# Optimization experiments

Hardware: AMD Instinct MI355X
Metric: run time of the kernel (lower is better)

Reference implementation:

```python
import jax, jax.numpy as jnp
import numpy as np

B, T, C = 8, 2048, 1024  # micro_bsz, seq_len, n_embd (== complexsize)


def setup_inputs() -> dict:
    key = jax.random.key(0)
    ks = jax.random.split(key, 6)
    w = lambda k, shape: (jax.random.normal(k, shape, dtype=jnp.float32) * 0.02)
    return {
        "x": jax.random.normal(ks[0], (B, T, C), dtype=jnp.float32),
        "Wk": w(ks[1], (2 * C, C)),      # key: n_embd -> 2*n_embd (no bias)
        "Wa": w(ks[2], (C, 2 * C)),      # activation: 2*n_embd -> n_embd (no bias)
        "Wf": w(ks[3], (2, C, C)),       # WaveNet filter conv, kernel=2, WIO layout
        "Wg": w(ks[4], (2, C, C)),       # WaveNet gate conv, kernel=2, WIO layout
        "Wo": w(ks[5], (C, C)),          # WaveNet 1x1 output projection
    }


def _causal_conv(x, W):
    # x: [B,T,Cin], W: [K,Cin,Cout]; left-pad K-1 for causality
    return jax.lax.conv_general_dilated(
        x, W, window_strides=(1,), padding=[(W.shape[0] - 1, 0)],
        dimension_numbers=("NWC", "WIO", "NWC"))


def _wavenet_short(x, Wf, Wg, Wo):
    # undialated gated WaveNet unit: tanh(conv_f(x)) * sigmoid(conv_g(x)) -> 1x1 proj
    h = jnp.tanh(_causal_conv(x, Wf)) * jax.nn.sigmoid(_causal_conv(x, Wg))
    return h @ Wo.T


def reference(x, Wk, Wa, Wf, Wg, Wo):
    Bx, Tx, Cx = x.shape
    k = (x @ Wk.T).reshape(Bx, Tx, Cx, 2)                 # [B,T,C,2]
    cv = jax.lax.complex(k[..., 0], k[..., 1])            # view_as_complex -> [B,T,C]
    scale = jax.lax.cummax(jnp.abs(cv), axis=1)           # running max of magnitude
    cv2 = cv / scale.astype(cv.dtype)                      # normalize magnitude <= 1
    kv = jnp.cumprod(cv2, axis=1)                          # complex cumulative product
    re = jnp.stack([kv.real, kv.imag], axis=-1).reshape(Bx, Tx, 2 * Cx)  # view_as_real
    return (re @ Wa.T) * _wavenet_short(x * scale, Wf, Wg, Wo)
```

## Files before the change

### kernel.cpp

```cpp
#include <hip/hip_runtime.h>
#include <cmath>

#define T_SEQ 2048
#define C_DIM 1024
#define BM 128
#define BN 128
#define BK 32

typedef unsigned short u16;
typedef unsigned int u32;
typedef short bf16x8 __attribute__((ext_vector_type(8)));
typedef _Float16 f16x8 __attribute__((ext_vector_type(8)));
typedef float f32x4 __attribute__((ext_vector_type(4)));
typedef unsigned short u16x8 __attribute__((ext_vector_type(8)));

#define AS1 __attribute__((address_space(1)))
#define AS3 __attribute__((address_space(3)))

__device__ __forceinline__ u16 f2bf(float f) {
    u32 u = __builtin_bit_cast(u32, f);
    u32 r = u + 0x7fffu + ((u >> 16) & 1u);
    return (u16)(r >> 16);
}
__device__ __forceinline__ u16 f2h(float f) {
    return __builtin_bit_cast(u16, (_Float16)f);
}
__device__ __forceinline__ float h2f(u16 h) {
    return (float)__builtin_bit_cast(_Float16, h);
}
__device__ __forceinline__ void gl_lds16(const void* g, void* l) {
    __builtin_amdgcn_global_load_lds((const AS1 u32*)g, (AS3 u32*)l, 16, 0, 0);
}

__device__ __forceinline__ int xcd_swz(int lin, int nwg) {
    return (lin & 7) * (nwg >> 3) + (lin >> 3);
}

template<int ASTAGE, int EPI, int DT>
__global__ __launch_bounds__(256)
void mfma_gemm(const void* __restrict__ Abase, const u16* __restrict__ B0,
               void* __restrict__ Cout, int M, int N, int K)
{
    __shared__ u16 lds[2 * 2 * 4096];
    const int tid  = threadIdx.x;
    const int lane = tid & 63;
    const int wid  = tid >> 6;
    const int wr = wid >> 1, wc = wid & 1;
    const int gx = gridDim.x;
    const int lin = xcd_swz(blockIdx.x + gx * blockIdx.y, gx * gridDim.y);
    const int m0 = (lin / gx) * BM;
    const int n0 = (lin % gx) * BN;
    const int NT = K / BK;

    f32x4 acc[4][4] = {};

    auto stage = [&](int it, int buf) {
        const int k0 = it * BK;
        u16* base = &lds[buf * 8192];
        #pragma unroll
        for (int i = 0; i < 2; ++i) {
            const int chunk = wid + 4 * i;
            const int rloc  = chunk * 16 + (lane >> 2);
            const int slot  = (lane & 3) ^ ((rloc >> 1) & 3);
            gl_lds16(B0 + (size_t)(n0 + rloc) * K + k0 + slot * 8,
                     base + 4096 + chunk * 512);
        }
        if constexpr (ASTAGE == 0) {
            const u16* Ap = (const u16*)Abase;
            #pragma unroll
            for (int i = 0; i < 2; ++i) {
                const int chunk = wid + 4 * i;
                const int rloc  = chunk * 16 + (lane >> 2);
                const int slot = (lane & 3) ^ ((rloc >> 1) & 3);
                gl_lds16(Ap + (size_t)(m0 + rloc) * K + k0 + slot * 8,
                         base + chunk * 512);
            }
        } else {
            const float* Af = (const float*)Abase;
            const int r = tid >> 1, h = tid & 1;
            const float* src = Af + (size_t)(m0 + r) * K + k0 + h * 16;
            const float4 q0 = ((const float4*)src)[0];
            const float4 q1 = ((const float4*)src)[1];
            const float4 q2 = ((const float4*)src)[2];
            const float4 q3 = ((const float4*)src)[3];
            float v[16] = {q0.x,q0.y,q0.z,q0.w, q1.x,q1.y,q1.z,q1.w,
                           q2.x,q2.y,q2.z,q2.w, q3.x,q3.y,q3.z,q3.w};
            const int rb = r * 32;
            #pragma unroll
            for (int s2 = 0; s2 < 2; ++s2) {
                const int slot = 2 * h + s2;
                const int sp = slot ^ ((r >> 1) & 3);
                u16x8 w;
                #pragma unroll
                for (int j = 0; j < 8; ++j) w[j] = f2bf(v[s2 * 8 + j]);
                *(u16x8*)&base[rb + sp * 8] = w;
            }
        }
    };

    auto compute = [&](int buf) {
        const u16* base = &lds[buf * 8192];
        if constexpr (DT == 0) {
            bf16x8 a[4], b[4];
            #pragma unroll
            for (int f = 0; f < 4; ++f) {
                const int row = wr * 64 + f * 16 + (lane & 15);
                const int sp  = ((lane >> 4) & 3) ^ ((row >> 1) & 3);
                a[f] = *(const bf16x8*)&base[row * 32 + sp * 8];
                const int rowb = wc * 64 + f * 16 + (lane & 15);
                const int spb  = ((lane >> 4) & 3) ^ ((rowb >> 1) & 3);
                b[f] = *(const bf16x8*)&base[4096 + rowb * 32 + spb * 8];
            }
            #pragma unroll
            for (int fm = 0; fm < 4; ++fm)
                #pragma unroll
                for (int fn = 0; fn < 4; ++fn)
                    acc[fm][fn] = __builtin_amdgcn_mfma_f32_16x16x32_bf16(a[fm], b[fn], acc[fm][fn], 0, 0, 0);
        } else {
            f16x8 a[4], b[4];
            #pragma unroll
            for (int f = 0; f < 4; ++f) {
                const int row = wr * 64 + f * 16 + (lane & 15);
                const int sp  = ((lane >> 4) & 3) ^ ((row >> 1) & 3);
                a[f] = *(const f16x8*)&base[row * 32 + sp * 8];
                const int rowb = wc * 64 + f * 16 + (lane & 15);
                const int spb  = ((lane >> 4) & 3) ^ ((rowb >> 1) & 3);
                b[f] = *(const f16x8*)&base[4096 + rowb * 32 + spb * 8];
            }
            #pragma unroll
            for (int fm = 0; fm < 4; ++fm)
                #pragma unroll
                for (int fn = 0; fn < 4; ++fn)
                    acc[fm][fn] = __builtin_amdgcn_mfma_f32_16x16x32_f16(a[fm], b[fn], acc[fm][fn], 0, 0, 0);
        }
    };

    stage(0, 0);
    int cur = 0;
    for (int it = 0; it < NT; ++it) {
        __syncthreads();
        if (it + 1 < NT) stage(it + 1, cur ^ 1);
        compute(cur);
        cur ^= 1;
    }

    const int crow0 = m0 + wr * 64 + ((lane >> 4) << 2);
    const int ccol  = n0 + wc * 64 + (lane & 15);
    #pragma unroll
    for (int fm = 0; fm < 4; ++fm)
        #pragma unroll
        for (int fn = 0; fn < 4; ++fn)
            #pragma unroll
            for (int r = 0; r < 4; ++r) {
                const size_t idx = (size_t)(crow0 + fm * 16 + r) * N + ccol + fn * 16;
                if constexpr (EPI == 0)      ((float*)Cout)[idx] = acc[fm][fn][r];
                else if constexpr (EPI == 1) ((float*)Cout)[idx] *= acc[fm][fn][r];
                else                         ((u16*)Cout)[idx] = f2h(acc[fm][fn][r]);
            }
}

__global__ __launch_bounds__(256)
void conv_gate(const u16* __restrict__ A, const u16* __restrict__ Wfgt,
               u16* __restrict__ H, int M)
{
    constexpr int KIT = C_DIM / BK;
    constexpr int NT  = 2 * KIT;
    __shared__ u16 lds[2 * 3 * 4096];
    const int tid  = threadIdx.x;
    const int lane = tid & 63;
    const int wid  = tid >> 6;
    const int wr = wid >> 1, wc = wid & 1;
    const int gx = gridDim.x;
    const int lin = xcd_swz(blockIdx.x + gx * blockIdx.y, gx * gridDim.y);
    const int m0 = (lin / gx) * BM;
    const int n0 = (lin % gx) * BN;

    f32x4 accF[4][4] = {};
    f32x4 accG[4][4] = {};

    auto stage = [&](int it, int buf) {
        const int p  = it / KIT;
        const int k0 = (it - p * KIT) * BK;
        u16* base = &lds[buf * 12288];
        const u16* BF = Wfgt + (size_t)p * 2 * C_DIM * C_DIM;
        const u16* BG = BF + (size_t)C_DIM * C_DIM;
        const int sh = (p == 0) ? 1 : 0;
        #pragma unroll
        for (int i = 0; i < 2; ++i) {
            const int chunk = wid + 4 * i;
            const int rloc  = chunk * 16 + (lane >> 2);
            const int slot  = (lane & 3) ^ ((rloc >> 1) & 3);
            int grow = m0 + rloc - sh;
            if (grow < 0) grow = 0;
            gl_lds16(A + (size_t)grow * C_DIM + k0 + slot * 8,
                     base + chunk * 512);
            gl_lds16(BF + (size_t)(n0 + rloc) * C_DIM + k0 + slot * 8,
                     base + 4096 + chunk * 512);
            gl_lds16(BG + (size_t)(n0 + rloc) * C_DIM + k0 + slot * 8,
                     base + 8192 + chunk * 512);
        }
    };

    auto compute = [&](int buf) {
        const u16* base = &lds[buf * 12288];
        bf16x8 a[4], bf[4], bg[4];
        #pragma unroll
        for (int f = 0; f < 4; ++f) {
            const int row = wr * 64 + f * 16 + (lane & 15);
            const int sp  = ((lane >> 4) & 3) ^ ((row >> 1) & 3);
            a[f] = *(const bf16x8*)&base[row * 32 + sp * 8];
            const int rowb = wc * 64 + f * 16 + (lane & 15);
            const int spb  = ((lane >> 4) & 3) ^ ((rowb >> 1) & 3);
            bf[f] = *(const bf16x8*)&base[4096 + rowb * 32 + spb * 8];
            bg[f] = *(const bf16x8*)&base[8192 + rowb * 32 + spb * 8];
        }
        #pragma unroll
        for (int fm = 0; fm < 4; ++fm)
            #pragma unroll
            for (int fn = 0; fn < 4; ++fn) {
                accF[fm][fn] = __builtin_amdgcn_mfma_f32_16x16x32_bf16(a[fm], bf[fn], accF[fm][fn], 0, 0, 0);
                accG[fm][fn] = __builtin_amdgcn_mfma_f32_16x16x32_bf16(a[fm], bg[fn], accG[fm][fn], 0, 0, 0);
            }
    };

    stage(0, 0);
    int cur = 0;
    for (int it = 0; it < NT; ++it) {
        __syncthreads();
        if ((it / KIT) == 0 && (m0 % T_SEQ) == 0) {
            if (tid < 4) {
                u16x8 z = {0,0,0,0,0,0,0,0};
                *(u16x8*)&lds[cur * 12288 + tid * 8] = z;
            }
            __syncthreads();
        }
        if (it + 1 < NT) stage(it + 1, cur ^ 1);
        compute(cur);
        cur ^= 1;
    }

    const int crow0 = m0 + wr * 64 + ((lane >> 4) << 2);
    const int ccol  = n0 + wc * 64 + (lane & 15);
    #pragma unroll
    for (int fm = 0; fm < 4; ++fm)
        #pragma unroll
        for (int fn = 0; fn < 4; ++fn)
            #pragma unroll
            for (int r = 0; r < 4; ++r) {
                const float fv = accF[fm][fn][r];
                const float gv = accG[fm][fn][r];
                const float th = 1.0f - 2.0f / (expf(2.0f * fv) + 1.0f);
                const float sg = 1.0f / (1.0f + expf(-gv));
                H[(size_t)(crow0 + fm * 16 + r) * C_DIM + ccol + fn * 16] = f2bf(th * sg);
            }
}

#define SSEG 32
#define SCHB 32
#define SSL (T_SEQ / SSEG)

__global__ __launch_bounds__(1024, 1)
void scan_kernel(u16* __restrict__ kq, const float* __restrict__ x,
                 u16* __restrict__ yb)
{
    __shared__ float  lmax[SSEG][SCHB];
    __shared__ float2 lprod[SSEG][SCHB];
    const int blk = blockIdx.x;
    const int b   = blk >> 5;
    const int c0  = (blk & 31) * SCHB;
    const int ch  = threadIdx.x & (SCHB - 1);
    const int seg = threadIdx.x >> 5;
    const int c   = c0 + ch;
    const int t0  = seg * SSL;
    const size_t baseh = (size_t)b * T_SEQ * 2048 + 2 * c + (size_t)t0 * 2048;
    const size_t base1 = (size_t)b * T_SEQ * C_DIM + c + (size_t)t0 * C_DIM;

    float m2 = 0.f;
    {
        size_t idx = baseh;
        for (int t = 0; t < SSL; ++t) {
            const u32 v = *(const u32*)&kq[idx];
            const float re = h2f((u16)(v & 0xffffu));
            const float im = h2f((u16)(v >> 16));
            m2 = fmaxf(m2, re * re + im * im);
            idx += 2048;
        }
    }
    lmax[seg][ch] = sqrtf(m2);
    __syncthreads();
    #pragma unroll
    for (int s = 1; s < SSEG; s <<= 1) {
        const float v = lmax[seg][ch];
        const float u = (seg >= s) ? lmax[seg - s][ch] : 0.f;
        __syncthreads();
        lmax[seg][ch] = fmaxf(v, u);
        __syncthreads();
    }
    const float premax = (seg > 0) ? lmax[seg - 1][ch] : 0.f;

    float pr = 1.f, pi = 0.f;
    float m = premax;
    {
        size_t idx = baseh, idx1 = base1;
        for (int t = 0; t < SSL; ++t) {
            const u32 v = *(const u32*)&kq[idx];
            const float re = h2f((u16)(v & 0xffffu));
            const float im = h2f((u16)(v >> 16));
            m = fmaxf(m, sqrtf(re * re + im * im));
            const float inv = 1.f / m;
            const float r0 = re * inv, r1 = im * inv;
            const float nr = pr * r0 - pi * r1;
            const float ni = pr * r1 + pi * r0;
            pr = nr; pi = ni;
            yb[idx1] = f2bf(x[idx1] * m);
            idx += 2048; idx1 += C_DIM;
        }
    }
    lprod[seg][ch] = make_float2(pr, pi);
    __syncthreads();
    #pragma unroll
    for (int s = 1; s < SSEG; s <<= 1) {
        const float2 v = lprod[seg][ch];
        const float2 u = (seg >= s) ? lprod[seg - s][ch] : make_float2(1.f, 0.f);
        __syncthreads();
        lprod[seg][ch] = make_float2(u.x * v.x - u.y * v.y,
                                     u.x * v.y + u.y * v.x);
        __syncthreads();
    }
    float ppr = 1.f, ppi = 0.f;
    if (seg > 0) { const float2 pp = lprod[seg - 1][ch]; ppr = pp.x; ppi = pp.y; }

    pr = 1.f; pi = 0.f;
    m = premax;
    {
        size_t idx = baseh;
        for (int t = 0; t < SSL; ++t) {
            const u32 v = *(const u32*)&kq[idx];
            const float re = h2f((u16)(v & 0xffffu));
            const float im = h2f((u16)(v >> 16));
            m = fmaxf(m, sqrtf(re * re + im * im));
            const float inv = 1.f / m;
            const float r0 = re * inv, r1 = im * inv;
            const float nr = pr * r0 - pi * r1;
            const float ni = pr * r1 + pi * r0;
            pr = nr; pi = ni;
            const float fr = ppr * nr - ppi * ni;
            const float fi = ppr * ni + ppi * nr;
            *(u32*)&kq[idx] = ((u32)f2bf(fi) << 16) | (u32)f2bf(fr);
            idx += 2048;
        }
    }
}

__global__ void cvt_bf16(const float* __restrict__ src, u16* __restrict__ dst, int n)
{
    const int i = (blockIdx.x * blockDim.x + threadIdx.x) * 4;
    if (i >= n) return;
    const float4 v = *(const float4*)&src[i];
    ushort4 o;
    o.x = f2bf(v.x); o.y = f2bf(v.y); o.z = f2bf(v.z); o.w = f2bf(v.w);
    *(ushort4*)&dst[i] = o;
}

__global__ void cvt_f16(const float* __restrict__ src, u16* __restrict__ dst, int n)
{
    const int i = (blockIdx.x * blockDim.x + threadIdx.x) * 4;
    if (i >= n) return;
    const float4 v = *(const float4*)&src[i];
    ushort4 o;
    o.x = f2h(v.x); o.y = f2h(v.y); o.z = f2h(v.z); o.w = f2h(v.w);
    *(ushort4*)&dst[i] = o;
}

__global__ __launch_bounds__(256)
void wtrans(const float* __restrict__ Wf, const float* __restrict__ Wg,
            u16* __restrict__ dst)
{
    __shared__ float tile[64][65];
    const int z = blockIdx.z;
    const float* src = ((z < 2) ? Wf : Wg) + (size_t)(z & 1) * C_DIM * C_DIM;
    u16* d = dst + (size_t)(z & 1) * (2 * C_DIM) * C_DIM
                 + ((z < 2) ? (size_t)0 : (size_t)C_DIM * C_DIM);
    const int k0 = blockIdx.x * 64;
    const int n0 = blockIdx.y * 64;
    const int tx = threadIdx.x & 63, ty = threadIdx.x >> 6;
    #pragma unroll
    for (int i = 0; i < 16; ++i) {
        const int r = ty + i * 4;
        tile[r][tx] = src[(size_t)(k0 + r) * C_DIM + n0 + tx];
    }
    __syncthreads();
    #pragma unroll
    for (int i = 0; i < 16; ++i) {
        const int r = ty + i * 4;
        d[(size_t)(n0 + r) * C_DIM + k0 + tx] = f2bf(tile[tx][r]);
    }
}

extern "C" void kernel_launch(void* const* d_in, const int* in_sizes, int n_in,
                              void* d_out, int out_size, void* d_ws, size_t ws_size,
                              hipStream_t stream)
{
    const float* x  = (const float*)d_in[0];
    const float* Wk = (const float*)d_in[1];
    const float* Wa = (const float*)d_in[2];
    const float* Wf = (const float*)d_in[3];
    const float* Wg = (const float*)d_in[4];
    const float* Wo = (const float*)d_in[5];
    float* out = (float*)d_out;

    const int M = 8 * T_SEQ;
    u16* kq   = (u16*)d_ws;
    u16* yb   = (u16*)((char*)d_ws + 67108864ull);
    u16* hb   = (u16*)((char*)d_ws + 100663296ull);
    u16* Wkh  = (u16*)((char*)d_ws + 134217728ull);
    u16* Wab  = Wkh + 2048 * 1024;
    u16* Wfgt = Wab + 2048 * 1024;
    u16* Wob  = Wfgt + 2ull * 2048 * 1024;

    cvt_f16 <<<(2048 * 1024 / 4 + 255) / 256, 256, 0, stream>>>(Wk, Wkh, 2048 * 1024);
    cvt_bf16<<<(2048 * 1024 / 4 + 255) / 256, 256, 0, stream>>>(Wa, Wab, 2048 * 1024);
    cvt_bf16<<<(1024 * 1024 / 4 + 255) / 256, 256, 0, stream>>>(Wo, Wob, 1024 * 1024);
    wtrans  <<<dim3(16, 16, 4), 256, 0, stream>>>(Wf, Wg, Wfgt);
    cvt_f16 <<<(M * 1024 / 4) / 256, 256, 0, stream>>>(x, yb, M * 1024);

    mfma_gemm<0, 2, 1><<<dim3(2048 / BN, M / BM), 256, 0, stream>>>(
        yb, Wkh, kq, M, 2048, 1024);

    scan_kernel<<<256, 1024, 0, stream>>>(kq, x, yb);

    mfma_gemm<0, 0, 0><<<dim3(1024 / BN, M / BM), 256, 0, stream>>>(
        kq, Wab, out, M, 1024, 2048);

    conv_gate<<<dim3(1024 / BN, M / BM), 256, 0, stream>>>(yb, Wfgt, hb, M);

    mfma_gemm<0, 1, 0><<<dim3(1024 / BN, M / BM), 256, 0, stream>>>(
        hb, Wob, out, M, 1024, 1024);
}
```

Baseline: 506.1 us.

## Fuse Wa and Wo GEMMs into one dual-accumulator kernel with product epilogue

The two final GEMMs (the kv@Wa projection and the h@Wo projection) become a single kernel that accumulates both products in registers and writes their elementwise product once. This drops the fp32 write of the first result and the read-modify-write of the second. The scan now reads x from the fp16 copy already in yb instead of the fp32 input, which cuts global traffic. The cost is doubled accumulator registers, which may lower occupancy or cause spills, and the scaled x is now built from fp16-rounded x.

```diff
diff --git a/kernel.cpp b/kernel.cpp
--- a/kernel.cpp
+++ b/kernel.cpp
@@ -28,6 +28,9 @@
 __device__ __forceinline__ float h2f(u16 h) {
     return (float)__builtin_bit_cast(_Float16, h);
 }
+__device__ __forceinline__ float bf2f(u16 h) {
+    return __builtin_bit_cast(float, (u32)h << 16);
+}
 __device__ __forceinline__ void gl_lds16(const void* g, void* l) {
     __builtin_amdgcn_global_load_lds((const AS1 u32*)g, (AS3 u32*)l, 16, 0, 0);
 }
@@ -36,9 +39,9 @@
     return (lin & 7) * (nwg >> 3) + (lin >> 3);
 }
 
-template<int ASTAGE, int EPI, int DT>
+template<int EPI, int DT>
 __global__ __launch_bounds__(256)
-void mfma_gemm(const void* __restrict__ Abase, const u16* __restrict__ B0,
+void mfma_gemm(const u16* __restrict__ Ap, const u16* __restrict__ B0,
                void* __restrict__ Cout, int M, int N, int K)
 {
     __shared__ u16 lds[2 * 2 * 4096];
@@ -64,37 +67,8 @@
             const int slot  = (lane & 3) ^ ((rloc >> 1) & 3);
             gl_lds16(B0 + (size_t)(n0 + rloc) * K + k0 + slot * 8,
                      base + 4096 + chunk * 512);
-        }
-        if constexpr (ASTAGE == 0) {
-            const u16* Ap = (const u16*)Abase;
-            #pragma unroll
-            for (int i = 0; i < 2; ++i) {
-                const int chunk = wid + 4 * i;
-                const int rloc  = chunk * 16 + (lane >> 2);
-                const int slot = (lane & 3) ^ ((rloc >> 1) & 3);
-                gl_lds16(Ap + (size_t)(m0 + rloc) * K + k0 + slot * 8,
-                         base + chunk * 512);
-            }
-        } else {
-            const float* Af = (const float*)Abase;
-            const int r = tid >> 1, h = tid & 1;
-            const float* src = Af + (size_t)(m0 + r) * K + k0 + h * 16;
-            const float4 q0 = ((const float4*)src)[0];
-            const float4 q1 = ((const float4*)src)[1];
-            const float4 q2 = ((const float4*)src)[2];
-            const float4 q3 = ((const float4*)src)[3];
-            float v[16] = {q0.x,q0.y,q0.z,q0.w, q1.x,q1.y,q1.z,q1.w,
-                           q2.x,q2.y,q2.z,q2.w, q3.x,q3.y,q3.z,q3.w};
-            const int rb = r * 32;
-            #pragma unroll
-            for (int s2 = 0; s2 < 2; ++s2) {
-                const int slot = 2 * h + s2;
-                const int sp = slot ^ ((r >> 1) & 3);
-                u16x8 w;
-                #pragma unroll
-                for (int j = 0; j < 8; ++j) w[j] = f2bf(v[s2 * 8 + j]);
-                *(u16x8*)&base[rb + sp * 8] = w;
-            }
+            gl_lds16(Ap + (size_t)(m0 + rloc) * K + k0 + slot * 8,
+                     base + chunk * 512);
         }
     };
 
@@ -153,9 +127,90 @@
             #pragma unroll
             for (int r = 0; r < 4; ++r) {
                 const size_t idx = (size_t)(crow0 + fm * 16 + r) * N + ccol + fn * 16;
-                if constexpr (EPI == 0)      ((float*)Cout)[idx] = acc[fm][fn][r];
-                else if constexpr (EPI == 1) ((float*)Cout)[idx] *= acc[fm][fn][r];
-                else                         ((u16*)Cout)[idx] = f2h(acc[fm][fn][r]);
+                if constexpr (EPI == 0) ((float*)Cout)[idx] = acc[fm][fn][r];
+                else                    ((u16*)Cout)[idx] = f2h(acc[fm][fn][r]);
+            }
+}
+
+__global__ __launch_bounds__(256)
+void dual_gemm(const u16* __restrict__ A1, const u16* __restrict__ B1, int K1,
+               const u16* __restrict__ A2, const u16* __restrict__ B2, int K2,
+               float* __restrict__ out, int M, int N)
+{
+    __shared__ u16 lds[2 * 2 * 4096];
+    const int tid  = threadIdx.x;
+    const int lane = tid & 63;
+    const int wid  = tid >> 6;
+    const int wr = wid >> 1, wc = wid & 1;
+    const int gx = gridDim.x;
+    const int lin = xcd_swz(blockIdx.x + gx * blockIdx.y, gx * gridDim.y);
+    const int m0 = (lin / gx) * BM;
+    const int n0 = (lin % gx) * BN;
+
+    f32x4 acc1[4][4] = {};
+    f32x4 acc2[4][4] = {};
+
+    auto stage = [&](const u16* Ap, const u16* Bp, int K, int it, int buf) {
+        const int k0 = it * BK;
+        u16* base = &lds[buf * 8192];
+        #pragma unroll
+        for (int i = 0; i < 2; ++i) {
+            const int chunk = wid + 4 * i;
+            const int rloc  = chunk * 16 + (lane >> 2);
+            const int slot  = (lane & 3) ^ ((rloc >> 1) & 3);
+            gl_lds16(Bp + (size_t)(n0 + rloc) * K + k0 + slot * 8,
+                     base + 4096 + chunk * 512);
+            gl_lds16(Ap + (size_t)(m0 + rloc) * K + k0 + slot * 8,
+                     base + chunk * 512);
+        }
+    };
+
+    auto compute = [&](int buf, f32x4 (&acc)[4][4]) {
+        const u16* base = &lds[buf * 8192];
+        bf16x8 a[4], b[4];
+        #pragma unroll
+        for (int f = 0; f < 4; ++f) {
+            const int row = wr * 64 + f * 16 + (lane & 15);
+            const int sp  = ((lane >> 4) & 3) ^ ((row >> 1) & 3);
+            a[f] = *(const bf16x8*)&base[row * 32 + sp * 8];
+            const int rowb = wc * 64 + f * 16 + (lane & 15);
+            const int spb  = ((lane >> 4) & 3) ^ ((rowb >> 1) & 3);
+            b[f] = *(const bf16x8*)&base[4096 + rowb * 32 + spb * 8];
+        }
+        #pragma unroll
+        for (int fm = 0; fm < 4; ++fm)
+            #pragma unroll
+            for (int fn = 0; fn < 4; ++fn)
+                acc[fm][fn] = __builtin_amdgcn_mfma_f32_16x16x32_bf16(a[fm], b[fn], acc[fm][fn], 0, 0, 0);
+    };
+
+    const int NT1 = K1 / BK, NT2 = K2 / BK;
+    stage(A1, B1, K1, 0, 0);
+    int cur = 0;
+    for (int it = 0; it < NT1; ++it) {
+        __syncthreads();
+        if (it + 1 < NT1) stage(A1, B1, K1, it + 1, cur ^ 1);
+        else              stage(A2, B2, K2, 0, cur ^ 1);
+        compute(cur, acc1);
+        cur ^= 1;
+    }
+    for (int it = 0; it < NT2; ++it) {
+        __syncthreads();
+        if (it + 1 < NT2) stage(A2, B2, K2, it + 1, cur ^ 1);
+        compute(cur, acc2);
+        cur ^= 1;
+    }
+
+    const int crow0 = m0 + wr * 64 + ((lane >> 4) << 2);
+    const int ccol  = n0 + wc * 64 + (lane & 15);
+    #pragma unroll
+    for (int fm = 0; fm < 4; ++fm)
+        #pragma unroll
+        for (int fn = 0; fn < 4; ++fn)
+            #pragma unroll
+            for (int r = 0; r < 4; ++r) {
+                const size_t idx = (size_t)(crow0 + fm * 16 + r) * N + ccol + fn * 16;
+                out[idx] = acc1[fm][fn][r] * acc2[fm][fn][r];
             }
 }
 
@@ -260,8 +315,7 @@
 #define SSL (T_SEQ / SSEG)
 
 __global__ __launch_bounds__(1024, 1)
-void scan_kernel(u16* __restrict__ kq, const float* __restrict__ x,
-                 u16* __restrict__ yb)
+void scan_kernel(u16* __restrict__ kq, u16* __restrict__ xyb)
 {
     __shared__ float  lmax[SSEG][SCHB];
     __shared__ float2 lprod[SSEG][SCHB];
@@ -312,7 +366,8 @@
             const float nr = pr * r0 - pi * r1;
             const float ni = pr * r1 + pi * r0;
             pr = nr; pi = ni;
-            yb[idx1] = f2bf(x[idx1] * m);
+            const float xv = h2f(xyb[idx1]);
+            xyb[idx1] = f2bf(xv * m);
             idx += 2048; idx1 += C_DIM;
         }
     }
@@ -424,16 +479,13 @@
     wtrans  <<<dim3(16, 16, 4), 256, 0, stream>>>(Wf, Wg, Wfgt);
     cvt_f16 <<<(M * 1024 / 4) / 256, 256, 0, stream>>>(x, yb, M * 1024);
 
-    mfma_gemm<0, 2, 1><<<dim3(2048 / BN, M / BM), 256, 0, stream>>>(
+    mfma_gemm<2, 1><<<dim3(2048 / BN, M / BM), 256, 0, stream>>>(
         yb, Wkh, kq, M, 2048, 1024);
 
-    scan_kernel<<<256, 1024, 0, stream>>>(kq, x, yb);
-
-    mfma_gemm<0, 0, 0><<<dim3(1024 / BN, M / BM), 256, 0, stream>>>(
-        kq, Wab, out, M, 1024, 2048);
+    scan_kernel<<<256, 1024, 0, stream>>>(kq, yb);
 
     conv_gate<<<dim3(1024 / BN, M / BM), 256, 0, stream>>>(yb, Wfgt, hb, M);
 
-    mfma_gemm<0, 1, 0><<<dim3(1024 / BN, M / BM), 256, 0, stream>>>(
-        hb, Wob, out, M, 1024, 1024);
-}
+    dual_gemm<<<dim3(1024 / BN, M / BM), 256, 0, stream>>>(
+        kq, Wab, 2048, hb, Wob, 1024, out, M, 1024);
+}
```

Result: faster. 473.0 us (-6.5%).
